# Kernel tuning notes

Measured on AMD Instinct MI355X. Metric: run time of the kernel, lower is better.

Reference implementation:

```python
import jax, jax.numpy as jnp
import numpy as np

# ---------------- config (from ObjectDetector source) ----------------
B = 2; IMG = 224; STRIDE = 32; FH = IMG // STRIDE          # 7x7 feature map
C_FEAT = 1024
SIZES = (32., 64., 128., 256., 512.); RATIOS = (0.5, 1.0, 2.0)
A = len(SIZES) * len(RATIOS)                                # 15 anchors/loc
NA = FH * FH * A                                            # 735 anchors/img
PRE_NMS = min(1000, NA); POST_NMS = min(1000, NA)           # testing config
RPN_NMS_T = 0.7; RPN_MIN_SIZE = 1e-3
NUM_CLASSES = 37
ROI_OUT = 7; ROI_SR = 2; ROI_SCALE = 1.0 / STRIDE
REP = 1024
SCORE_T = 0.05; DET_NMS_T = 0.5; DETS_PER_IMG = 100
CAND_K = 2048            # candidate cap before final batched NMS
MIN_SIZE_DET = 1e-2
BBOX_CLIP = float(np.log(1000.0 / 16.0))


def make_anchors():
    scales = np.array(SIZES, np.float32); ratios = np.array(RATIOS, np.float32)
    h_r = np.sqrt(ratios); w_r = 1.0 / h_r
    ws = (w_r[:, None] * scales[None, :]).reshape(-1)
    hs = (h_r[:, None] * scales[None, :]).reshape(-1)
    base = np.round(np.stack([-ws, -hs, ws, hs], 1) / 2.0)   # [A,4]
    sy, sx = np.meshgrid(np.arange(FH) * STRIDE, np.arange(FH) * STRIDE, indexing='ij')
    shifts = np.stack([sx.reshape(-1), sy.reshape(-1), sx.reshape(-1), sy.reshape(-1)], 1).astype(np.float32)
    return jnp.asarray((shifts[:, None, :] + base[None, :, :]).reshape(-1, 4))  # [NA,4] (H,W,A)


def conv(x, w, b, stride=1, pad=0):
    y = jax.lax.conv_general_dilated(x, w, (stride, stride), [(pad, pad)] * 2,
                                     dimension_numbers=('NCHW', 'OIHW', 'NCHW'))
    return y + b[None, :, None, None]


def decode_boxes(deltas, boxes, weights):
    wx, wy, ww, wh = weights
    w = boxes[..., 2] - boxes[..., 0]; h = boxes[..., 3] - boxes[..., 1]
    cx = boxes[..., 0] + 0.5 * w; cy = boxes[..., 1] + 0.5 * h
    dx = deltas[..., 0] / wx; dy = deltas[..., 1] / wy
    dw = jnp.minimum(deltas[..., 2] / ww, BBOX_CLIP)
    dh = jnp.minimum(deltas[..., 3] / wh, BBOX_CLIP)
    pcx = dx * w + cx; pcy = dy * h + cy
    pw = jnp.exp(dw) * w; ph = jnp.exp(dh) * h
    return jnp.stack([pcx - 0.5 * pw, pcy - 0.5 * ph, pcx + 0.5 * pw, pcy + 0.5 * ph], -1)


def clip_boxes(b):
    x = jnp.clip(b[..., 0::2], 0.0, float(IMG)); y = jnp.clip(b[..., 1::2], 0.0, float(IMG))
    return jnp.stack([x[..., 0], y[..., 0], x[..., 1], y[..., 1]], -1)


def box_iou(a, b):
    area_a = (a[:, 2] - a[:, 0]) * (a[:, 3] - a[:, 1])
    area_b = (b[:, 2] - b[:, 0]) * (b[:, 3] - b[:, 1])
    lt = jnp.maximum(a[:, None, :2], b[None, :, :2])
    rb = jnp.minimum(a[:, None, 2:], b[None, :, 2:])
    wh = jnp.clip(rb - lt, 0.0, None)
    inter = wh[..., 0] * wh[..., 1]
    return inter / jnp.maximum(area_a[:, None] + area_b[None, :] - inter, 1e-9)


def nms_keep(boxes, scores, thresh):
    """Greedy NMS; returns keep mask in original order (fixed shapes)."""
    n = boxes.shape[0]
    order = jnp.argsort(-scores)
    iou = box_iou(*(jax.lax.stop_gradient(boxes[order]),) * 2)
    idx = jnp.arange(n)
    def body(i, keep):
        sup = (iou[i] > thresh) & (idx > i) & keep[i]
        return keep & ~sup
    keep_sorted = jax.lax.fori_loop(0, n, body, jnp.ones(n, bool))
    return jnp.zeros(n, bool).at[order].set(keep_sorted)


def rpn_filter_one(obj_logits, deltas, anchors):
    # obj_logits [NA], deltas [NA,4] (detached, as in torchvision RPN)
    top_v, top_i = jax.lax.top_k(obj_logits, PRE_NMS)
    boxes = clip_boxes(decode_boxes(deltas[top_i], anchors[top_i], (1., 1., 1., 1.)))
    prob = jax.nn.sigmoid(top_v)
    ws = boxes[:, 2] - boxes[:, 0]; hs = boxes[:, 3] - boxes[:, 1]
    prob = jnp.where((ws >= RPN_MIN_SIZE) & (hs >= RPN_MIN_SIZE), prob, -1.0)
    prob = jnp.where(nms_keep(boxes, prob, RPN_NMS_T), prob, -1.0)
    sv, si = jax.lax.top_k(prob, POST_NMS)
    return boxes[si], sv > 0.0


def bilinear(f_hwc, ys, xs):
    # torchvision roi_align bilinear sampling; f_hwc [H,W,C], ys/xs [R,O]
    H, W, _ = f_hwc.shape
    vy = (ys >= -1.0) & (ys <= H); vx = (xs >= -1.0) & (xs <= W)
    y = jnp.clip(ys, 0.0, None); x = jnp.clip(xs, 0.0, None)
    y0 = jnp.minimum(jnp.floor(y).astype(jnp.int32), H - 1)
    x0 = jnp.minimum(jnp.floor(x).astype(jnp.int32), W - 1)
    y1 = jnp.minimum(y0 + 1, H - 1); x1 = jnp.minimum(x0 + 1, W - 1)
    y = jnp.where(y0 == H - 1, y0.astype(y.dtype), y)
    x = jnp.where(x0 == W - 1, x0.astype(x.dtype), x)
    ly = y - y0; lx = x - x0; hy = 1.0 - ly; hx = 1.0 - lx
    g = lambda yi, xi: f_hwc[yi[:, :, None], xi[:, None, :]]   # [R,O,O,C]
    val = ((hy[:, :, None] * hx[:, None, :])[..., None] * g(y0, x0)
         + (hy[:, :, None] * lx[:, None, :])[..., None] * g(y0, x1)
         + (ly[:, :, None] * hx[:, None, :])[..., None] * g(y1, x0)
         + (ly[:, :, None] * lx[:, None, :])[..., None] * g(y1, x1))
    return val * (vy[:, :, None] & vx[:, None, :])[..., None]


def roi_align_one(feat_chw, rois):
    # feat [C,H,W], rois [R,4] -> [R,C,7,7]; output_size=7, sampling_ratio=2, scale=1/32
    f = jnp.transpose(feat_chw, (1, 2, 0))
    x1 = rois[:, 0] * ROI_SCALE; y1 = rois[:, 1] * ROI_SCALE
    rw = jnp.maximum(rois[:, 2] * ROI_SCALE - x1, 1.0)
    rh = jnp.maximum(rois[:, 3] * ROI_SCALE - y1, 1.0)
    bw = rw / ROI_OUT; bh = rh / ROI_OUT
    grid = jnp.arange(ROI_OUT, dtype=jnp.float32)
    acc = 0.0
    for iy in range(ROI_SR):
        ys = y1[:, None] + (grid[None, :] + (iy + 0.5) / ROI_SR) * bh[:, None]
        for ix in range(ROI_SR):
            xs = x1[:, None] + (grid[None, :] + (ix + 0.5) / ROI_SR) * bw[:, None]
            acc = acc + bilinear(f, ys, xs)
    return jnp.transpose(acc / (ROI_SR * ROI_SR), (0, 3, 1, 2))


def postprocess_one(logits, box_deltas, proposals, roi_valid):
    R = logits.shape[0]
    scores = jax.nn.softmax(logits, -1)
    boxes = clip_boxes(decode_boxes(box_deltas.reshape(R, NUM_CLASSES, 4),
                                    proposals[:, None, :], (10., 10., 5., 5.)))
    boxes = boxes[:, 1:, :].reshape(-1, 4)       # drop background class
    scores = jnp.where(roi_valid[:, None], scores[:, 1:], 0.0).reshape(-1)
    labels = jnp.broadcast_to(jnp.arange(1, NUM_CLASSES)[None, :], (R, NUM_CLASSES - 1)).reshape(-1)
    ws = boxes[:, 2] - boxes[:, 0]; hs = boxes[:, 3] - boxes[:, 1]
    ok = (ws >= MIN_SIZE_DET) & (hs >= MIN_SIZE_DET) & (scores > SCORE_T)
    cs, ci = jax.lax.top_k(jnp.where(ok, scores, -1.0), CAND_K)
    cb = boxes[ci]; cl = labels[ci]
    off = cl.astype(cb.dtype) * (IMG + 1.0)      # batched (per-class) NMS trick
    keep = nms_keep(cb + off[:, None], cs, DET_NMS_T)
    tv, ti = jax.lax.top_k(jnp.where(keep, cs, -1.0), DETS_PER_IMG)
    valid = tv > 0.0
    out_boxes = jnp.where(valid[:, None], cb[ti], 0.0)
    out_scores = jnp.where(valid, tv, 0.0)
    out_labels = jnp.where(valid, cl[ti], 0).astype(out_boxes.dtype)
    return jnp.concatenate([out_boxes, out_scores[:, None], out_labels[:, None]], -1)  # [100,6]


def forward(images, params, anchors):
    (bb_w, bb_b, rpn_w, rpn_b, cls_w, cls_b, reg_w, reg_b,
     fc1_w, fc1_b, fc2_w, fc2_b, clsp_w, clsp_b, boxp_w, boxp_b) = params
    Bn = images.shape[0]
    feats = jax.nn.relu(conv(images, bb_w, bb_b, stride=STRIDE))        # [B,1024,7,7]
    t = jax.nn.relu(conv(feats, rpn_w, rpn_b, stride=1, pad=1))
    obj = jnp.transpose(conv(t, cls_w, cls_b), (0, 2, 3, 1)).reshape(Bn, -1)            # [B,NA]
    reg = jnp.transpose(conv(t, reg_w, reg_b).reshape(Bn, A, 4, FH, FH),
                        (0, 3, 4, 1, 2)).reshape(Bn, -1, 4)                              # [B,NA,4]
    obj_d = jax.lax.stop_gradient(obj); reg_d = jax.lax.stop_gradient(reg)  # RPN detaches
    proposals, roi_valid = jax.vmap(lambda o, d: rpn_filter_one(o, d, anchors))(obj_d, reg_d)
    pooled = jax.vmap(roi_align_one)(feats, proposals)                  # [B,R,1024,7,7]
    x = pooled.reshape(Bn * POST_NMS, -1)
    x = jax.nn.relu(x @ fc1_w.T + fc1_b)
    x = jax.nn.relu(x @ fc2_w.T + fc2_b)
    logits = (x @ clsp_w.T + clsp_b).reshape(Bn, POST_NMS, NUM_CLASSES)
    bdelt = (x @ boxp_w.T + boxp_b).reshape(Bn, POST_NMS, NUM_CLASSES * 4)
    return jax.vmap(postprocess_one)(logits, bdelt, proposals, roi_valid)  # [B,100,6]


def setup_inputs() -> dict:
    key = jax.random.key(0)
    ks = jax.random.split(key, 10)
    w = lambda k, shape, s=0.02: jax.random.normal(k, shape, jnp.float32) * s
    return {
        'images': jax.random.uniform(ks[0], (B, 1, IMG, IMG), jnp.float32),
        'bb_w': w(ks[1], (C_FEAT, 1, STRIDE, STRIDE)), 'bb_b': jnp.zeros((C_FEAT,), jnp.float32),
        'rpn_w': w(ks[2], (C_FEAT, C_FEAT, 3, 3)), 'rpn_b': jnp.zeros((C_FEAT,), jnp.float32),
        'cls_w': w(ks[3], (A, C_FEAT, 1, 1)), 'cls_b': jnp.zeros((A,), jnp.float32),
        'reg_w': w(ks[4], (4 * A, C_FEAT, 1, 1)), 'reg_b': jnp.zeros((4 * A,), jnp.float32),
        'fc1_w': w(ks[5], (REP, C_FEAT * ROI_OUT * ROI_OUT), 0.005), 'fc1_b': jnp.zeros((REP,), jnp.float32),
        'fc2_w': w(ks[6], (REP, REP)), 'fc2_b': jnp.zeros((REP,), jnp.float32),
        'clsp_w': w(ks[7], (NUM_CLASSES, REP)), 'clsp_b': jnp.zeros((NUM_CLASSES,), jnp.float32),
        'boxp_w': w(ks[8], (NUM_CLASSES * 4, REP)), 'boxp_b': jnp.zeros((NUM_CLASSES * 4,), jnp.float32),
    }


def reference(images, bb_w, bb_b, rpn_w, rpn_b, cls_w, cls_b, reg_w, reg_b,
              fc1_w, fc1_b, fc2_w, fc2_b, clsp_w, clsp_b, boxp_w, boxp_b):
    anchors = make_anchors()
    params = (bb_w, bb_b, rpn_w, rpn_b, cls_w, cls_b, reg_w, reg_b,
              fc1_w, fc1_b, fc2_w, fc2_b, clsp_w, clsp_b, boxp_w, boxp_b)
    return forward(images, params, anchors)
```

## Files before the change

kernel.cpp:

```cpp
#include <hip/hip_runtime.h>
#include <math.h>

#define NANCH 735
#define NCAND 26460
#define NCANDP 26624
#define BBCLIP 4.135166556742356f
#define KF1 4864
#define KHALF 2432

typedef short bf16x8 __attribute__((ext_vector_type(8)));
typedef float f32x4 __attribute__((ext_vector_type(4)));

__device__ __forceinline__ unsigned short f2b(float f) {
  unsigned int u = __float_as_uint(f);
  unsigned int r = (u >> 16) & 1u;
  u += 0x7fffu + r;
  return (unsigned short)(u >> 16);
}

__device__ __forceinline__ void anchor_of(int i, float* o) {
  int pos = i / 15, a = i % 15;
  int iy = pos / 7, ix = pos % 7;
  int rr = a / 5, sc = a % 5;
  double ratio = (rr == 0) ? 0.5 : (rr == 1 ? 1.0 : 2.0);
// ... 12 lines not shown

template<int NTOT, int NTH>
__device__ void bitonic_sort_sh(float* v, int* id) {
  const int t = threadIdx.x;
  for (int k = 2; k <= NTOT; k <<= 1) {
    for (int j = k >> 1; j > 0; j >>= 1) {
      for (int s = t; s < NTOT; s += NTH) {
        int p = s ^ j;
        if (p > s) {
          float v1 = v[s], v2 = v[p];
          int i1 = id[s], i2 = id[p];
          bool up = ((s & k) == 0);
          if (before_(v2, i2, v1, i1) == up) {
            v[s] = v2; id[s] = i2; v[p] = v1; id[p] = i1;
          }
        }
      }
      __syncthreads();
    }
  }
}

template<int NTOT, int NTH>
__device__ void bitonic_merge_sh(float* v, int* id) {
  const int t = threadIdx.x;
  for (int j = NTOT >> 1; j > 0; j >>= 1) {
    for (int s = t; s < NTOT; s += NTH) {
      int p = s ^ j;
      if (p > s) {
        float v1 = v[s], v2 = v[p];
        int i1 = id[s], i2 = id[p];
        if (before_(v2, i2, v1, i1)) {
          v[s] = v2; id[s] = i2; v[p] = v1; id[p] = i1;
        }
      }
    }
    __syncthreads();
  }
}

__global__ void k_im2col_bb(const float* __restrict__ images, unsigned short* __restrict__ patch) {
  int i = blockIdx.x * 256 + threadIdx.x;
  if (i >= 98 * 1024) return;
  int rowi = i >> 10, k = i & 1023;
  int b = rowi / 49, pos = rowi % 49;
  int oy = pos / 7, ox = pos % 7;
  int ky = k >> 5, kx = k & 31;
  patch[i] = f2b(images[((size_t)b * 224 + oy * 32 + ky) * 224 + ox * 32 + kx]);
}

__global__ void k_im2col_rpn(const unsigned short* __restrict__ bbh,
                             unsigned short* __restrict__ im2) {
  int i = blockIdx.x * 256 + threadIdx.x;
  if (i >= 98 * 9216) return;
  int rowi = i / 9216, k = i % 9216;
  int b = rowi / 49, pos = rowi % 49;
  int oy = pos / 7, ox = pos % 7;
  int ic = k / 9, kk = k % 9;
  int ky = kk / 3, kx = kk % 3;
  int y = oy + ky - 1, x = ox + kx - 1;
  unsigned short v = 0;
  if ((unsigned)y < 7u && (unsigned)x < 7u)
    v = bbh[((size_t)(b * 49 + y * 7 + x)) * 1024 + ic];
  im2[i] = v;
}

__global__ __launch_bounds__(256) void k_gemm_bf16(
    const unsigned short* __restrict__ A, int lda, int M,
    const unsigned short* __restrict__ B, int ldb,
    float* __restrict__ P, int N, int Kchunk,
    const int* __restrict__ nvalid)
{
  __shared__ __attribute__((aligned(16))) unsigned short As[2][128][40];
  __shared__ __attribute__((aligned(16))) unsigned short Bs[2][128][40];
  const int G = gridDim.x * gridDim.y * gridDim.z;
  int lid = blockIdx.x + gridDim.x * (blockIdx.y + gridDim.y * blockIdx.z);
  lid = (lid & 7) * (G >> 3) + (lid >> 3);
  const int bx = lid % gridDim.x;
  const int rest = lid / gridDim.x;
  const int by = rest % gridDim.y, bz = rest / gridDim.y;
  const int m0 = bx * 128, n0 = by * 128;
  if (nvalid) {
    int nv0 = nvalid[0], nv1 = nvalid[1];
    bool ok = (m0 < nv0) || ((m0 + 128 > NANCH) && (m0 < NANCH + nv1));
    if (!ok) return;
  }
  const int t = threadIdx.x;
  const int lane = t & 63, wid = t >> 6;
  const int wm = (wid >> 1) * 64, wn = (wid & 1) * 64;
  const size_t k0 = (size_t)bz * Kchunk;
  f32x4 acc[4][4];
#pragma unroll
  for (int i = 0; i < 4; ++i)
#pragma unroll
    for (int j = 0; j < 4; ++j) acc[i][j] = (f32x4){0.f, 0.f, 0.f, 0.f};
  const int r0 = t >> 2, c0 = (t & 3) * 8;
  const int fr = lane & 15, fk = (lane >> 4) * 8;
  const int gmA0 = m0 + r0, gmA1 = m0 + r0 + 64;
  const bool vA0 = gmA0 < M, vA1 = gmA1 < M;
  const unsigned short* pA0 = A + (size_t)gmA0 * lda + k0 + c0;
  const unsigned short* pA1 = A + (size_t)gmA1 * lda + k0 + c0;
  const unsigned short* pB0 = B + (size_t)(n0 + r0) * ldb + k0 + c0;
  const unsigned short* pB1 = B + (size_t)(n0 + r0 + 64) * ldb + k0 + c0;
  bf16x8 rA0 = {}, rA1 = {}, rB0, rB1;
  if (vA0) rA0 = *(const bf16x8*)pA0;
  if (vA1) rA1 = *(const bf16x8*)pA1;
  rB0 = *(const bf16x8*)pB0;
  rB1 = *(const bf16x8*)pB1;
  const int nt = Kchunk >> 5;
  int cur = 0;
  for (int it = 0; it < nt; ++it) {
    *(bf16x8*)&As[cur][r0][c0] = rA0;
    *(bf16x8*)&As[cur][r0 + 64][c0] = rA1;
    *(bf16x8*)&Bs[cur][r0][c0] = rB0;
    *(bf16x8*)&Bs[cur][r0 + 64][c0] = rB1;
    __syncthreads();
    if (it + 1 < nt) {
      size_t ofs = (size_t)(it + 1) * 32;
      rA0 = vA0 ? *(const bf16x8*)(pA0 + ofs) : (bf16x8){};
      rA1 = vA1 ? *(const bf16x8*)(pA1 + ofs) : (bf16x8){};
      rB0 = *(const bf16x8*)(pB0 + ofs);
      rB1 = *(const bf16x8*)(pB1 + ofs);
    }
    bf16x8 af[4], bg[4];
#pragma unroll
    for (int i = 0; i < 4; ++i) af[i] = *(const bf16x8*)&As[cur][wm + i * 16 + fr][fk];
#pragma unroll
    for (int j = 0; j < 4; ++j) bg[j] = *(const bf16x8*)&Bs[cur][wn + j * 16 + fr][fk];
#pragma unroll
    for (int i = 0; i < 4; ++i)
#pragma unroll
      for (int j = 0; j < 4; ++j)
        acc[i][j] = __builtin_amdgcn_mfma_f32_16x16x32_bf16(af[i], bg[j], acc[i][j], 0, 0, 0);
    cur ^= 1;
  }
  float* Pp = P + (size_t)bz * M * N;
#pragma unroll
  for (int i = 0; i < 4; ++i) {
#pragma unroll
    for (int r = 0; r < 4; ++r) {
      int gm = m0 + wm + i * 16 + (lane >> 4) * 4 + r;
      if (gm < M) {
#pragma unroll
        for (int j = 0; j < 4; ++j)
          Pp[(size_t)gm * N + n0 + wn + j * 16 + (lane & 15)] = acc[i][j][r];
      }
    }
  }
}

__global__ __launch_bounds__(256) void k_gemm_mb(
    const unsigned short* __restrict__ A,
    const unsigned short* __restrict__ W1p,
    unsigned short* __restrict__ Mbh)
{
  __shared__ __attribute__((aligned(16))) unsigned short As[2][128][40];
  __shared__ __attribute__((aligned(16))) unsigned short Bs[2][128][40];
  const int G = gridDim.x * gridDim.y * gridDim.z;
  int lid = blockIdx.x + gridDim.x * (blockIdx.y + gridDim.y * blockIdx.z);
  lid = (lid & 7) * (G >> 3) + (lid >> 3);
  const int rest = lid;
  const int by = rest % gridDim.y, p = rest / gridDim.y;
  const int n0 = by * 128;
  const int M = 98;
  const unsigned short* B = W1p + (size_t)p * 1048576;
  const int t = threadIdx.x;
  const int lane = t & 63, wid = t >> 6;
  const int wm = (wid >> 1) * 64, wn = (wid & 1) * 64;
  f32x4 acc[4][4];
#pragma unroll
  for (int i = 0; i < 4; ++i)
#pragma unroll
    for (int j = 0; j < 4; ++j) acc[i][j] = (f32x4){0.f, 0.f, 0.f, 0.f};
  const int r0 = t >> 2, c0 = (t & 3) * 8;
  const int fr = lane & 15, fk = (lane >> 4) * 8;
  int gA0 = r0; if (gA0 >= M) gA0 = M - 1;
  int gA1 = r0 + 64; if (gA1 >= M) gA1 = M - 1;
  const unsigned short* pA0 = A + (size_t)gA0 * 1024 + c0;
  const unsigned short* pA1 = A + (size_t)gA1 * 1024 + c0;
  const unsigned short* pB0 = B + (size_t)(n0 + r0) * 1024 + c0;
  const unsigned short* pB1 = B + (size_t)(n0 + r0 + 64) * 1024 + c0;
  bf16x8 rA0 = *(const bf16x8*)pA0;
  bf16x8 rA1 = *(const bf16x8*)pA1;
  bf16x8 rB0 = *(const bf16x8*)pB0;
  bf16x8 rB1 = *(const bf16x8*)pB1;
  const int nt = 1024 >> 5;
  int cur = 0;
  for (int it = 0; it < nt; ++it) {
    *(bf16x8*)&As[cur][r0][c0] = rA0;
    *(bf16x8*)&As[cur][r0 + 64][c0] = rA1;
    *(bf16x8*)&Bs[cur][r0][c0] = rB0;
    *(bf16x8*)&Bs[cur][r0 + 64][c0] = rB1;
    __syncthreads();
    if (it + 1 < nt) {
      size_t ofs = (size_t)(it + 1) * 32;
      rA0 = *(const bf16x8*)(pA0 + ofs);
      rA1 = *(const bf16x8*)(pA1 + ofs);
      rB0 = *(const bf16x8*)(pB0 + ofs);
      rB1 = *(const bf16x8*)(pB1 + ofs);
    }
    bf16x8 af[4], bg[4];
#pragma unroll
    for (int i = 0; i < 4; ++i) af[i] = *(const bf16x8*)&As[cur][wm + i * 16 + fr][fk];
#pragma unroll
    for (int j = 0; j < 4; ++j) bg[j] = *(const bf16x8*)&Bs[cur][wn + j * 16 + fr][fk];
#pragma unroll
    for (int i = 0; i < 4; ++i)
#pragma unroll
      for (int j = 0; j < 4; ++j)
        acc[i][j] = __builtin_amdgcn_mfma_f32_16x16x32_bf16(af[i], bg[j], acc[i][j], 0, 0, 0);
    cur ^= 1;
  }
  unsigned short* Pp = Mbh + (size_t)p * 98 * 1024;
#pragma unroll
  for (int i = 0; i < 4; ++i) {
#pragma unroll
    for (int r = 0; r < 4; ++r) {
      int gm = wm + i * 16 + (lane >> 4) * 4 + r;
      if (gm < M) {
#pragma unroll
        for (int j = 0; j < 4; ++j)
          Pp[(size_t)gm * 1024 + n0 + wn + j * 16 + (lane & 15)] = f2b(acc[i][j][r]);
      }
    }
  }
}

__global__ __launch_bounds__(256) void k_mtrans(const unsigned short* __restrict__ Mbh,
                                                unsigned short* __restrict__ Bmat)
{
  __shared__ unsigned short tile[98][129];
  const int p = blockIdx.x, n0 = blockIdx.y * 128;
  const int t = threadIdx.x;
  for (int j = t; j < 98 * 128; j += 256) {
    int q = j >> 7, nl = j & 127;
    tile[q][nl] = Mbh[((size_t)p * 98 + q) * 1024 + n0 + nl];
  }
  __syncthreads();
  for (int j = t; j < 128 * 98; j += 256) {
    int nl = j / 98, q2 = j % 98;
    int bb = q2 >= 49 ? 1 : 0;
    int col = bb * KHALF + p * 49 + (q2 - bb * 49);
    Bmat[(size_t)(n0 + nl) * KF1 + col] = tile[q2][nl];
  }
  if (p == 0) {
    for (int j = t; j < 128 * 62; j += 256) {
      int nl = j / 62, e = j % 62;
      int bb = e >= 31 ? 1 : 0;
      int col = bb * KHALF + 2401 + (e - bb * 31);
      Bmat[(size_t)(n0 + nl) * KF1 + col] = 0;
    }
  }
}

__global__ __launch_bounds__(256) void k_gbuild(const float* __restrict__ props,
                                                unsigned short* __restrict__ Gmat)
{
#pragma clang fp contract(off)
  int rg = blockIdx.x;
  int b = rg / NANCH;
  __shared__ float g[KF1];
  int t = threadIdx.x;
  for (int j = t; j < KF1; j += 256) g[j] = 0.f;
  __syncthreads();
  if (t < 49) {
    const float* roi = props + (size_t)rg * 4;
    int p = t, oy = p / 7, ox = p % 7;
    float x1 = roi[0] * 0.03125f, y1 = roi[1] * 0.03125f;
    float rw = fmaxf(roi[2] * 0.03125f - x1, 1.f);
    float rh = fmaxf(roi[3] * 0.03125f - y1, 1.f);
    float bw = rw / 7.f, bh = rh / 7.f;
    float* gb = g + b * KHALF + p * 49;
    for (int iy = 0; iy < 2; ++iy) {
      for (int ix = 0; ix < 2; ++ix) {
        float ys = y1 + ((float)oy + ((float)iy + 0.5f) * 0.5f) * bh;
        float xs = x1 + ((float)ox + ((float)ix + 0.5f) * 0.5f) * bw;
        bool vy = (ys >= -1.f) && (ys <= 7.f);
        bool vx = (xs >= -1.f) && (xs <= 7.f);
        float yc = fmaxf(ys, 0.f), xc = fmaxf(xs, 0.f);
        int y0 = min((int)floorf(yc), 6), x0 = min((int)floorf(xc), 6);
        int y1i = min(y0 + 1, 6), x1i = min(x0 + 1, 6);
        if (y0 == 6) yc = 6.f;
        if (x0 == 6) xc = 6.f;
        float ly = yc - (float)y0, lx = xc - (float)x0;
        float hy = 1.f - ly, hx = 1.f - lx;
        float vm = (vy && vx) ? 0.25f : 0.f;
        gb[y0 * 7 + x0]   += hy * hx * vm;
        gb[y0 * 7 + x1i]  += hy * lx * vm;
        gb[y1i * 7 + x0]  += ly * hx * vm;
        gb[y1i * 7 + x1i] += ly * lx * vm;
      }
    }
  }
  __syncthreads();
  unsigned short* Gr = Gmat + (size_t)rg * KF1;
  for (int j = t; j < KF1; j += 256) Gr[j] = f2b(g[j]);
}

__global__ void k_reduce(const float* __restrict__ P, float* __restrict__ dst,
                         unsigned short* __restrict__ dst16,
                         int S, int M, int N, const float* __restrict__ bias, int flags)
{
  size_t i = (size_t)blockIdx.x * 256 + threadIdx.x;
  size_t tot = (size_t)M * N;
  if (i >= tot) return;
  float v = (flags & 1) ? 0.f : dst[i];
  for (int s = 0; s < S; ++s) v += P[(size_t)s * tot + i];
  if (flags & 2) v += bias[i % (size_t)N];
  if (flags & 4) v = fmaxf(v, 0.f);
  if (!(flags & 16)) dst[i] = v;
  if (flags & 8) dst16[i] = f2b(v);
}

__global__ void k_f2b3(const float* __restrict__ s1, unsigned short* __restrict__ d1,
                       const float* __restrict__ s2, unsigned short* __restrict__ d2,
                       const float* __restrict__ s3, unsigned short* __restrict__ d3)
{
  int i = (blockIdx.x * 256 + threadIdx.x) * 4;
  const float* s; unsigned short* d; int off;
  if (i < 1048576) { s = s1; d = d1; off = i; }
  else if (i < 2097152) { s = s2; d = d2; off = i - 1048576; }
  else if (i < 11534336) { s = s3; d = d3; off = i - 2097152; }
  else return;
  float4 v = *(const float4*)(s + off);
  ushort4 o;
  o.x = f2b(v.x); o.y = f2b(v.y); o.z = f2b(v.z); o.w = f2b(v.w);
  *(ushort4*)(d + off) = o;
}

__global__ __launch_bounds__(256) void k_w1perm2(const float* __restrict__ w,
                                                 unsigned short* __restrict__ o)
{
  __shared__ unsigned short tile[128 * 50];
  const int n = blockIdx.x, ct = blockIdx.y;
  const float* src = w + (size_t)n * 50176 + (size_t)ct * 128 * 49;
  const int t = threadIdx.x;
  for (int i = t; i < 6272; i += 256) {
    int cl = i / 49, p = i % 49;
    tile[cl * 50 + p] = f2b(src[i]);
  }
  __syncthreads();
  for (int j = t; j < 6272; j += 256) {
    int p = j >> 7, cl = j & 127;
    o[((size_t)p * 1024 + n) * 1024 + (size_t)ct * 128 + cl] = tile[cl * 50 + p];
  }
}

__global__ __launch_bounds__(256) void k_rpn_head(
    const float* __restrict__ tmn, const float* __restrict__ cls_w,
    const float* __restrict__ cls_b, const float* __restrict__ reg_w,
    const float* __restrict__ reg_b, float* __restrict__ obj, float* __restrict__ reg)
{
  int blk = blockIdx.x;
  __shared__ float col[1024];
  const float* row = tmn + (size_t)blk * 1024;
  for (int i = threadIdx.x; i < 1024; i += 256) col[i] = row[i];
  __syncthreads();
  int b = blk / 49, pos = blk % 49;
  for (int o = threadIdx.x; o < 75; o += 256) {
    const float* w = (o < 15) ? (cls_w + (size_t)o * 1024) : (reg_w + (size_t)(o - 15) * 1024);
    float s = 0.f;
    for (int k = 0; k < 1024; ++k) s = fmaf(col[k], w[k], s);
    if (o < 15) {
      obj[(size_t)b * NANCH + pos * 15 + o] = s + cls_b[o];
    } else {
      int c = o - 15, a = c >> 2, d = c & 3;
      reg[((size_t)b * NANCH + pos * 15 + a) * 4 + d] = s + reg_b[c];
    }
  }
}

__global__ __launch_bounds__(1024) void k_rpn_prep(
    const float* __restrict__ obj, const float* __restrict__ reg,
    float* __restrict__ bxp, float* __restrict__ pnms)
{
#pragma clang fp contract(off)
  const int b = blockIdx.x, t = threadIdx.x;
  __shared__ float sval[1024];
  __shared__ float vo1[1024];
  __shared__ int o1a[1024];
  __shared__ int wtv[16];
  __shared__ int wti[16];
  sval[t] = (t < NANCH) ? obj[(size_t)b * NANCH + t] : -INFINITY;
  __syncthreads();
  {
    float v = sval[t];
    int rank = 0;
    for (int j = 0; j < NANCH; ++j) {
      float u = sval[j];
      rank += (u > v) || (u == v && j < t);
    }
    if (t < NANCH) { vo1[rank] = v; o1a[rank] = t; }
  }
  __syncthreads();
  float x1 = 0.f, y1 = 0.f, x2 = 0.f, y2 = 0.f, prob = -1.f;
  bool flag = false;
  if (t < NANCH) {
    int ai = o1a[t];
    const float* d = reg + ((size_t)b * NANCH + ai) * 4;
    float an[4];
    anchor_of(ai, an);
    float aw = an[2] - an[0], ah = an[3] - an[1];
    float acx = an[0] + 0.5f * aw, acy = an[1] + 0.5f * ah;
    float dw = fminf(d[2], BBCLIP), dh = fminf(d[3], BBCLIP);
    float pcx = d[0] * aw + acx, pcy = d[1] * ah + acy;
    float pw = expf(dw) * aw, ph = expf(dh) * ah;
    x1 = pcx - 0.5f * pw; y1 = pcy - 0.5f * ph;
    x2 = pcx + 0.5f * pw; y2 = pcy + 0.5f * ph;
    x1 = fminf(fmaxf(x1, 0.f), 224.f);
    y1 = fminf(fmaxf(y1, 0.f), 224.f);
    x2 = fminf(fmaxf(x2, 0.f), 224.f);
    y2 = fminf(fmaxf(y2, 0.f), 224.f);
    flag = (x2 - x1 >= 1e-3f) && (y2 - y1 >= 1e-3f);
    prob = 1.f / (1.f + expf(-vo1[t]));
  }
  bool iflag = (t < NANCH) && !flag;
  unsigned long long balv = __ballot(flag);
  unsigned long long bali = __ballot(iflag);
  int lane = t & 63, w = t >> 6;
  if (lane == 0) { wtv[w] = __popcll(balv); wti[w] = __popcll(bali); }
  __syncthreads();
  int nval = 0, basev = 0, basei = 0;
  for (int k = 0; k < 16; ++k) {
    int cv = wtv[k], ci = wti[k];
    nval += cv;
    if (k < w) { basev += cv; basei += ci; }
  }
  if (t < NANCH) {
    unsigned long long lm = (1ull << lane) - 1;
    int pos = flag ? (basev + __popcll(balv & lm))
                   : (nval + basei + __popcll(bali & lm));
    float* o = bxp + ((size_t)b * NANCH + pos) * 4;
    o[0] = x1; o[1] = y1; o[2] = x2; o[3] = y2;
    pnms[(size_t)b * NANCH + pos] = flag ? prob : -1.f;
  }
}

__global__ __launch_bounds__(256) void k_rpn_mask(
    const float* __restrict__ bxp, unsigned long long* __restrict__ rmask)
{
#pragma clang fp contract(off)
  int blk = blockIdx.x;
  int b = blk / 35;
  int row = (blk % 35) * 21 + (int)(threadIdx.x / 12);
  int w = threadIdx.x % 12;
  if (threadIdx.x >= 252 || row >= NANCH) return;
  const float* a = bxp + ((size_t)b * NANCH + row) * 4;
  float a0 = a[0], a1 = a[1], a2 = a[2], a3 = a[3];
  float aarea = (a2 - a0) * (a3 - a1);
  int l0 = w * 64;
  int l1 = (l0 + 64 < NANCH) ? l0 + 64 : NANCH;
  int ls = (l0 > row + 1) ? l0 : row + 1;
  unsigned long long bits = 0ull;
  for (int l = ls; l < l1; ++l) {
    const float* q = bxp + ((size_t)b * NANCH + l) * 4;
    float b0 = q[0], b1 = q[1], b2 = q[2], b3 = q[3];
    float barea = (b2 - b0) * (b3 - b1);
    float ix1 = fmaxf(a0, b0), iy1 = fmaxf(a1, b1);
    float ix2 = fminf(a2, b2), iy2 = fminf(a3, b3);
    float iw = fmaxf(ix2 - ix1, 0.f), ih = fmaxf(iy2 - iy1, 0.f);
    float inter = iw * ih;
    float iou = inter / fmaxf(aarea + barea - inter, 1e-9f);
    if (iou > 0.7f) bits |= 1ull << (l & 63);
  }
  rmask[((size_t)b * NANCH + row) * 12 + w] = bits;
}

__global__ __launch_bounds__(1024) void k_rpn_fin(
    const float* __restrict__ bxp, const float* __restrict__ pnms,
    const unsigned long long* __restrict__ rmask,
    float* __restrict__ props, int* __restrict__ meta)
{
  const int b = blockIdx.x, t = threadIdx.x;
  __shared__ unsigned long long smask[NANCH * 12];
  __shared__ float sp[1024];
  __shared__ unsigned long long keepw[12];
  __shared__ int wtot[16];
  for (int i = t; i < NANCH * 12; i += 1024)
    smask[i] = rmask[(size_t)b * NANCH * 12 + i];
  sp[t] = (t < NANCH) ? pnms[(size_t)b * NANCH + t] : -1.f;
  __syncthreads();
  if (t < 64) {
    unsigned long long kl = (t < 12) ? ~0ull : 0ull;
    for (int i = 0; i < NANCH; ++i) {
      unsigned long long kw = __shfl(kl, i >> 6);
      unsigned long long m = (t < 12) ? smask[i * 12 + t] : 0ull;
      bool on = (kw >> (i & 63)) & 1ull;
      kl &= on ? ~m : ~0ull;
    }
    if (t < 12) keepw[t] = kl;
  }
  __syncthreads();
  bool flag = false;
  if (t < NANCH) {
    bool kp = (keepw[t >> 6] >> (t & 63)) & 1ull;
    flag = kp && (sp[t] > 0.f);
  }
  unsigned long long bal = __ballot(flag);
  int lane = t & 63, w = t >> 6;
  if (lane == 0) wtot[w] = __popcll(bal);
  __syncthreads();
  int base = 0, tot = 0;
  for (int k = 0; k < 16; ++k) { int c = wtot[k]; if (k < w) base += c; tot += c; }
  if (flag) {
    int pos = base + __popcll(bal & ((1ull << lane) - 1));
    const float* src = bxp + ((size_t)b * NANCH + t) * 4;
    float* o = props + ((size_t)b * NANCH + pos) * 4;
    o[0] = src[0]; o[1] = src[1]; o[2] = src[2]; o[3] = src[3];
  }
  if (t == 0) meta[b] = tot;
}

__global__ __launch_bounds__(256) void k_headcand(
    const float* __restrict__ h2, const float* __restrict__ cw,
    const float* __restrict__ cb, const float* __restrict__ bw_,
    const float* __restrict__ bb_, const int* __restrict__ meta,
    const float* __restrict__ props,
    float* __restrict__ cscore, float* __restrict__ cbox)
{
#pragma clang fp contract(off)
  int rg = blockIdx.x;
  int b = rg / NANCH, r = rg % NANCH;
  float* cs = cscore + (size_t)b * NCANDP;
  float* cbx = cbox + (size_t)b * NCANDP * 4;
  int base = r * 36;
  if (r >= meta[b]) {
    int j = threadIdx.x;
    if (j < 36) {
      cs[base + j] = -1.f;
      float* q = cbx + (size_t)(base + j) * 4;
      q[0] = 0.f; q[1] = 0.f; q[2] = 0.f; q[3] = 0.f;
    }
    return;
  }
  __shared__ float row[1024];
  __shared__ float lg[37];
  __shared__ float bd[148];
  __shared__ float mxsum[2];
  for (int i = threadIdx.x; i < 1024; i += 256) row[i] = h2[(size_t)rg * 1024 + i];
  __syncthreads();
  for (int o = threadIdx.x; o < 185; o += 256) {
    const float* w = (o < 37) ? (cw + (size_t)o * 1024) : (bw_ + (size_t)(o - 37) * 1024);
    float s = 0.f;
    for (int k = 0; k < 1024; ++k) s = fmaf(row[k], w[k], s);
    if (o < 37) lg[o] = s + cb[o];
    else bd[o - 37] = s + bb_[o - 37];
  }
  __syncthreads();
  if (threadIdx.x == 0) {
    float mx = lg[0];
    for (int c = 1; c < 37; ++c) mx = fmaxf(mx, lg[c]);
    float sum = 0.f;
    for (int c = 0; c < 37; ++c) sum += expf(lg[c] - mx);
    mxsum[0] = mx; mxsum[1] = sum;
  }
  __syncthreads();
  int c = threadIdx.x + 1;
  if (c <= 36) {
    const float* roi = props + (size_t)rg * 4;
    float rw = roi[2] - roi[0], rh = roi[3] - roi[1];
    float rcx = roi[0] + 0.5f * rw, rcy = roi[1] + 0.5f * rh;
    const float* d = bd + c * 4;
    float dx = d[0] / 10.f, dy = d[1] / 10.f;
    float dw = fminf(d[2] / 5.f, BBCLIP), dh = fminf(d[3] / 5.f, BBCLIP);
    float pcx = dx * rw + rcx, pcy = dy * rh + rcy;
    float pw = expf(dw) * rw, ph = expf(dh) * rh;
    float x1 = pcx - 0.5f * pw, y1 = pcy - 0.5f * ph;
    float x2 = pcx + 0.5f * pw, y2 = pcy + 0.5f * ph;
    x1 = fminf(fmaxf(x1, 0.f), 224.f);
    y1 = fminf(fmaxf(y1, 0.f), 224.f);
    x2 = fminf(fmaxf(x2, 0.f), 224.f);
    y2 = fminf(fmaxf(y2, 0.f), 224.f);
    float sc = expf(lg[c] - mxsum[0]) / mxsum[1];
    bool ok = ((x2 - x1) >= 1e-2f) && ((y2 - y1) >= 1e-2f) && (sc > 0.05f);
    cs[base + c - 1] = ok ? sc : -1.f;
    float* q = cbx + (size_t)(base + c - 1) * 4;
    q[0] = x1; q[1] = y1; q[2] = x2; q[3] = y2;
  }
}

__global__ __launch_bounds__(1024) void k_top2048(
    const float* __restrict__ cscore,
    float* __restrict__ sel_score, int* __restrict__ sel_cidx,
    int* __restrict__ meta)
{
  const int b = blockIdx.x, t = threadIdx.x;
  __shared__ float Lv[2048]; __shared__ int Li[2048];
  __shared__ float Cv[2048]; __shared__ int Ci[2048];
  __shared__ int cnt;
  const float* cs = cscore + (size_t)b * NCANDP;
  if (t == 0) cnt = 0;
  __syncthreads();
  for (int gi = t; gi < NCAND; gi += 1024) {
    float v = cs[gi];
    if (v > 0.f) {
      int p = atomicAdd(&cnt, 1);
      if (p < 2048) { Cv[p] = v; Ci[p] = gi; }
    }
  }
  __syncthreads();
  int npos = cnt;
  if (npos <= 2048) {
    for (int h = 0; h < 2; ++h) {
      int p = h * 1024 + t;
      if (p < npos) {
        float v = Cv[p]; int id = Ci[p];
        int rank = 0;
        for (int j = 0; j < npos; ++j) {
          float u = Cv[j]; int ju = Ci[j];
          rank += (u > v) || (u == v && ju < id);
        }
        sel_score[b * 2048 + rank] = v;
        sel_cidx[b * 2048 + rank] = id;
      }
      if (p >= npos && p < 2048) {
        sel_score[b * 2048 + p] = -1.f;
        sel_cidx[b * 2048 + p] = 0;
      }
    }
    if (t == 0) meta[2 + b] = npos;
    return;
  }
  for (int chunk = 0; chunk < 13; ++chunk) {
    for (int s = t; s < 2048; s += 1024) {
      int gi = chunk * 2048 + s;
      Cv[s] = (gi < NCAND) ? cs[gi] : -INFINITY;
      Ci[s] = gi;
    }
    __syncthreads();
    bitonic_sort_sh<2048, 1024>(Cv, Ci);
    if (chunk == 0) {
      for (int s = t; s < 2048; s += 1024) { Lv[s] = Cv[s]; Li[s] = Ci[s]; }
      __syncthreads();
    } else {
      for (int s = t; s < 2048; s += 1024) {
        float cv = Cv[2047 - s]; int ci = Ci[2047 - s];
        if (before_(cv, ci, Lv[s], Li[s])) { Lv[s] = cv; Li[s] = ci; }
      }
      __syncthreads();
      bitonic_merge_sh<2048, 1024>(Lv, Li);
    }
  }
  for (int s = t; s < 2048; s += 1024) {
    sel_score[b * 2048 + s] = Lv[s];
    sel_cidx[b * 2048 + s] = Li[s];
  }
  if (t == 0) meta[2 + b] = 2048;
}

__global__ void k_detmask(const int* __restrict__ sel_cidx,
                          const float* __restrict__ cbox,
                          const int* __restrict__ meta,
                          unsigned long long* __restrict__ dmask)
{
#pragma clang fp contract(off)
  int blk = blockIdx.x;
  int b = blk >> 8, row0 = (blk & 255) * 8;
  int npos = meta[2 + b];
  if (row0 >= npos) return;
  int t = threadIdx.x;
  int i = row0 + (t >> 5), w = t & 31;
  if (i >= npos) return;
  int ci = sel_cidx[b * 2048 + i];
  const float* bp = cbox + ((size_t)b * NCANDP + ci) * 4;
  float off = (float)(ci % 36 + 1) * 225.f;
  float a0 = bp[0] + off, a1 = bp[1] + off, a2 = bp[2] + off, a3 = bp[3] + off;
  float aarea = (a2 - a0) * (a3 - a1);
  unsigned long long bits = 0ull;
  int l0 = w * 64;
  int l1 = (l0 + 64 < npos) ? l0 + 64 : npos;
  int ls = (l0 > i + 1) ? l0 : i + 1;
  for (int l = ls; l < l1; ++l) {
    int cl = sel_cidx[b * 2048 + l];
    const float* q = cbox + ((size_t)b * NCANDP + cl) * 4;
    float o2 = (float)(cl % 36 + 1) * 225.f;
    float b0 = q[0] + o2, b1 = q[1] + o2, b2 = q[2] + o2, b3 = q[3] + o2;
    float barea = (b2 - b0) * (b3 - b1);
    float ix1 = fmaxf(a0, b0), iy1 = fmaxf(a1, b1);
    float ix2 = fminf(a2, b2), iy2 = fminf(a3, b3);
    float iw = fmaxf(ix2 - ix1, 0.f), ih = fmaxf(iy2 - iy1, 0.f);
    float inter = iw * ih;
    float iou = inter / fmaxf(aarea + barea - inter, 1e-9f);
    if (iou > 0.5f) bits |= 1ull << (l & 63);
  }
  dmask[((size_t)b * 2048 + i) * 32 + w] = bits;
}

__global__ __launch_bounds__(1024) void k_final(
    const float* __restrict__ sel_score, const int* __restrict__ sel_cidx,
    const float* __restrict__ cbox, const unsigned long long* __restrict__ dmask,
    const int* __restrict__ meta, float* __restrict__ out)
{
  const int b = blockIdx.x, t = threadIdx.x;
  __shared__ unsigned long long keepw[32];
  __shared__ float sv[2048];
  __shared__ float kv[2048]; __shared__ int ks[2048];
  __shared__ int wtot[32];
  int npos = meta[2 + b];
  for (int h = 0; h < 2; ++h) {
    int s = h * 1024 + t;
    sv[s] = sel_score[b * 2048 + s];
  }
  __syncthreads();
  if (t < 64) {
    unsigned long long kl = (t < 32) ? ~0ull : 0ull;
    for (int i = 0; i < npos; ++i) {
      unsigned long long kw = __shfl(kl, i >> 6);
      unsigned long long m = (t < 32) ? dmask[((size_t)b * 2048 + i) * 32 + t] : 0ull;
      bool on = (kw >> (i & 63)) & 1ull;
      kl &= on ? ~m : ~0ull;
    }
    if (t < 32) keepw[t] = kl;
  }
  __syncthreads();
  const int lane = t & 63, w = t >> 6;
  int s0 = t;
  bool f0 = ((keepw[s0 >> 6] >> (s0 & 63)) & 1ull) && (sv[s0] > 0.f);
  unsigned long long bal0 = __ballot(f0);
  if (lane == 0) wtot[w] = __popcll(bal0);
  int s1 = 1024 + t;
  bool f1 = ((keepw[s1 >> 6] >> (s1 & 63)) & 1ull) && (sv[s1] > 0.f);
  unsigned long long bal1 = __ballot(f1);
  if (lane == 0) wtot[16 + w] = __popcll(bal1);
  __syncthreads();
  int nk = 0, base0 = 0, base1 = 0;
  for (int k = 0; k < 32; ++k) {
    int c = wtot[k];
    if (k < w) base0 += c;
    if (k < 16 + w) base1 += c;
    nk += c;
  }
  int p0 = -1, p1 = -1;
  if (f0) { p0 = base0 + __popcll(bal0 & ((1ull << lane) - 1)); kv[p0] = sv[s0]; ks[p0] = s0; }
  if (f1) { p1 = base1 + __popcll(bal1 & ((1ull << lane) - 1)); kv[p1] = sv[s1]; ks[p1] = s1; }
  __syncthreads();
  if (f0) {
    float v = sv[s0]; int rank = 0;
    for (int j = 0; j < nk; ++j) { float u = kv[j]; int ju = ks[j]; rank += (u > v) || (u == v && ju < s0); }
    if (rank < 100) {
      int ci = sel_cidx[b * 2048 + s0];
      const float* bp = cbox + ((size_t)b * NCANDP + ci) * 4;
      float* o = out + ((size_t)b * 100 + rank) * 6;
      o[0] = bp[0]; o[1] = bp[1]; o[2] = bp[2]; o[3] = bp[3];
      o[4] = v; o[5] = (float)(ci % 36 + 1);
    }
  }
  if (f1) {
    float v = sv[s1]; int rank = 0;
    for (int j = 0; j < nk; ++j) { float u = kv[j]; int ju = ks[j]; rank += (u > v) || (u == v && ju < s1); }
    if (rank < 100) {
      int ci = sel_cidx[b * 2048 + s1];
      const float* bp = cbox + ((size_t)b * NCANDP + ci) * 4;
      float* o = out + ((size_t)b * 100 + rank) * 6;
      o[0] = bp[0]; o[1] = bp[1]; o[2] = bp[2]; o[3] = bp[3];
      o[4] = v; o[5] = (float)(ci % 36 + 1);
    }
  }
  if (t < 100 && t >= nk) {
    float* o = out + ((size_t)b * 100 + t) * 6;
    o[0] = 0.f; o[1] = 0.f; o[2] = 0.f; o[3] = 0.f; o[4] = 0.f; o[5] = 0.f;
  }
}

extern "C" void kernel_launch(void* const* d_in, const int* in_sizes, int n_in,
                              void* d_out, int out_size, void* d_ws, size_t ws_size,
                              hipStream_t stream)
{
  (void)in_sizes; (void)n_in; (void)out_size; (void)ws_size;
  const float* images = (const float*)d_in[0];
  const float* bb_w   = (const float*)d_in[1];
  const float* bb_b   = (const float*)d_in[2];
  const float* rpn_w  = (const float*)d_in[3];
  const float* rpn_b  = (const float*)d_in[4];
  const float* cls_w  = (const float*)d_in[5];
  const float* cls_b  = (const float*)d_in[6];
  const float* reg_w  = (const float*)d_in[7];
  const float* reg_b  = (const float*)d_in[8];
  const float* fc1_w  = (const float*)d_in[9];
  const float* fc1_b  = (const float*)d_in[10];
  const float* fc2_w  = (const float*)d_in[11];
  const float* fc2_b  = (const float*)d_in[12];
  const float* clsp_w = (const float*)d_in[13];
  const float* clsp_b = (const float*)d_in[14];
  const float* boxp_w = (const float*)d_in[15];
  const float* boxp_b = (const float*)d_in[16];
  float* out = (float*)d_out;
  char* ws = (char*)d_ws;

  size_t off = 0;
  auto alloc = [&](size_t bytes) -> size_t {
    size_t o = off; off = (off + bytes + 255) & ~(size_t)255; return o;
  };
  size_t o_patch = alloc(98ull * 1024 * 2);
  size_t o_bbC   = alloc(98ull * 1024 * 4);
  size_t o_bbh   = alloc(98ull * 1024 * 2);
  size_t o_t     = alloc(98ull * 1024 * 4);
  size_t o_im2   = alloc(98ull * 9216 * 2);
  size_t o_obj   = alloc(1470ull * 4);
  size_t o_reg   = alloc(1470ull * 16);
  size_t o_props = alloc(1470ull * 16);
  size_t o_bxp   = alloc(1470ull * 16);
  size_t o_pnms  = alloc(1470ull * 4);
  size_t o_rm    = alloc(1470ull * 12 * 8);
  size_t o_meta  = alloc(256);
  size_t o_y1    = alloc(1470ull * 1024 * 4);
  size_t o_y2    = alloc(1470ull * 1024 * 4);
  size_t o_cs    = alloc(2ull * NCANDP * 4);
  size_t o_cb    = alloc(2ull * NCANDP * 16);
  size_t o_ss    = alloc(2ull * 2048 * 4);
  size_t o_sc    = alloc(2ull * 2048 * 4);
  size_t o_dm    = alloc(2ull * 2048 * 32 * 8);
  size_t o_w0b   = alloc(1048576ull * 2);
  size_t o_w3b   = alloc(9437184ull * 2);
  size_t o_w1p   = alloc(51380224ull * 2);
  size_t o_mbh   = alloc(49ull * 98 * 1024 * 2);
  size_t o_bmat  = alloc(1024ull * KF1 * 2);
  size_t o_gmat  = alloc(1470ull * KF1 * 2);
  size_t o_w2b   = alloc(1048576ull * 2);
  size_t o_y1b   = alloc(1470ull * 1024 * 2);
  size_t o_P     = alloc(32ull * 98 * 1024 * 4 > 4ull * 1470 * 1024 * 4
                         ? 32ull * 98 * 1024 * 4 : 4ull * 1470 * 1024 * 4);

  unsigned short* patchb = (unsigned short*)(ws + o_patch);
  float* bbC   = (float*)(ws + o_bbC);
  unsigned short* bbh = (unsigned short*)(ws + o_bbh);
  float* tb    = (float*)(ws + o_t);
  unsigned short* im2b = (unsigned short*)(ws + o_im2);
  float* objb  = (float*)(ws + o_obj);
  float* regb  = (float*)(ws + o_reg);
  float* props = (float*)(ws + o_props);
  float* bxp   = (float*)(ws + o_bxp);
  float* pnms  = (float*)(ws + o_pnms);
  unsigned long long* rmb = (unsigned long long*)(ws + o_rm);
  int*   meta  = (int*)(ws + o_meta);
  float* y1    = (float*)(ws + o_y1);
  float* y2    = (float*)(ws + o_y2);
  float* csb   = (float*)(ws + o_cs);
  float* cbb   = (float*)(ws + o_cb);
  float* ssb   = (float*)(ws + o_ss);
  int*   scb   = (int*)(ws + o_sc);
  unsigned long long* dmb = (unsigned long long*)(ws + o_dm);
  unsigned short* w0b = (unsigned short*)(ws + o_w0b);
  unsigned short* w3b = (unsigned short*)(ws + o_w3b);
  unsigned short* w1p = (unsigned short*)(ws + o_w1p);
  unsigned short* mbh = (unsigned short*)(ws + o_mbh);
  unsigned short* bmat = (unsigned short*)(ws + o_bmat);
  unsigned short* gmat = (unsigned short*)(ws + o_gmat);
  unsigned short* w2b = (unsigned short*)(ws + o_w2b);
  unsigned short* y1b = (unsigned short*)(ws + o_y1b);
  float* Pb    = (float*)(ws + o_P);

  k_w1perm2<<<dim3(1024, 8), 256, 0, stream>>>(fc1_w, w1p);
  k_f2b3<<<11264, 256, 0, stream>>>(fc2_w, w2b, bb_w, w0b, rpn_w, w3b);
  k_im2col_bb<<<392, 256, 0, stream>>>(images, patchb);
  k_gemm_bf16<<<dim3(1, 8, 8), 256, 0, stream>>>(patchb, 1024, 98, w0b, 1024, Pb, 1024, 128, nullptr);
  k_reduce<<<392, 256, 0, stream>>>(Pb, bbC, bbh, 8, 98, 1024, bb_b, 31);
  k_gemm_mb<<<dim3(1, 8, 49), 256, 0, stream>>>(bbh, w1p, mbh);
  k_mtrans<<<dim3(49, 8), 256, 0, stream>>>(mbh, bmat);
  k_im2col_rpn<<<3528, 256, 0, stream>>>(bbh, im2b);
  k_gemm_bf16<<<dim3(1, 8, 32), 256, 0, stream>>>(im2b, 9216, 98, w3b, 9216, Pb, 1024, 288, nullptr);
  k_reduce<<<392, 256, 0, stream>>>(Pb, tb, nullptr, 32, 98, 1024, rpn_b, 7);
  k_rpn_head<<<98, 256, 0, stream>>>(tb, cls_w, cls_b, reg_w, reg_b, objb, regb);
  k_rpn_prep<<<2, 1024, 0, stream>>>(objb, regb, bxp, pnms);
  k_rpn_mask<<<70, 256, 0, stream>>>(bxp, rmb);
  k_rpn_fin<<<2, 1024, 0, stream>>>(bxp, pnms, rmb, props, meta);
  k_gbuild<<<1470, 256, 0, stream>>>(props, gmat);
  k_gemm_bf16<<<dim3(12, 8, 4), 256, 0, stream>>>(gmat, KF1, 1470, bmat, KF1, Pb, 1024, 1216, meta);
  k_reduce<<<5880, 256, 0, stream>>>(Pb, y1, y1b, 4, 1470, 1024, fc1_b, 31);
  k_gemm_bf16<<<dim3(12, 8, 2), 256, 0, stream>>>(y1b, 1024, 1470, w2b, 1024, Pb, 1024, 512, meta);
  k_reduce<<<5880, 256, 0, stream>>>(Pb, y2, nullptr, 2, 1470, 1024, fc2_b, 7);
  k_headcand<<<1470, 256, 0, stream>>>(y2, clsp_w, clsp_b, boxp_w, boxp_b, meta, props, csb, cbb);
  k_top2048<<<2, 1024, 0, stream>>>(csb, ssb, scb, meta);
  k_detmask<<<512, 256, 0, stream>>>(scb, cbb, meta, dmb);
  k_final<<<2, 1024, 0, stream>>>(ssb, scb, cbb, dmb, meta, out);
}
```

Measured before the change: 457.8 us.

## Fuse fc1 transpose into GEMM epilogue and run box head as bf16 MFMA GEMM

The fc1 weight-projection GEMM now stages its bf16 output in shared memory and writes the transposed Bmat layout directly, which removes the separate k_mtrans kernel and its intermediate buffer. The class and box predictor heads, previously a scalar per-ROI dot-product loop in k_headcand, are now a padded 256-column bf16 MFMA GEMM with split-K. The bf16 head weights are produced in the existing conversion kernel, and a light per-ROI kernel finishes softmax and box decoding. This trades fp32 head precision for bf16 and adds an extra GEMM launch, while the strided column writes in the fused epilogue may be poorly coalesced.

```diff
diff --git a/kernel.cpp b/kernel.cpp
--- a/kernel.cpp
+++ b/kernel.cpp
@@ -188,10 +188,11 @@
 __global__ __launch_bounds__(256) void k_gemm_mb(
     const unsigned short* __restrict__ A,
     const unsigned short* __restrict__ W1p,
-    unsigned short* __restrict__ Mbh)
+    unsigned short* __restrict__ Bmat)
 {
   __shared__ __attribute__((aligned(16))) unsigned short As[2][128][40];
   __shared__ __attribute__((aligned(16))) unsigned short Bs[2][128][40];
+  __shared__ unsigned short tile[98][130];
   const int G = gridDim.x * gridDim.y * gridDim.z;
   int lid = blockIdx.x + gridDim.x * (blockIdx.y + gridDim.y * blockIdx.z);
   lid = (lid & 7) * (G >> 3) + (lid >> 3);
@@ -247,7 +248,7 @@
         acc[i][j] = __builtin_amdgcn_mfma_f32_16x16x32_bf16(af[i], bg[j], acc[i][j], 0, 0, 0);
     cur ^= 1;
   }
-  unsigned short* Pp = Mbh + (size_t)p * 98 * 1024;
+  __syncthreads();
 #pragma unroll
   for (int i = 0; i < 4; ++i) {
 #pragma unroll
@@ -256,32 +257,19 @@
       if (gm < M) {
 #pragma unroll
         for (int j = 0; j < 4; ++j)
-          Pp[(size_t)gm * 1024 + n0 + wn + j * 16 + (lane & 15)] = f2b(acc[i][j][r]);
+          tile[gm][wn + j * 16 + (lane & 15)] = f2b(acc[i][j][r]);
       }
     }
   }
-}
-
-__global__ __launch_bounds__(256) void k_mtrans(const unsigned short* __restrict__ Mbh,
-                                                unsigned short* __restrict__ Bmat)
-{
-  __shared__ unsigned short tile[98][129];
-  const int p = blockIdx.x, n0 = blockIdx.y * 128;
-  const int t = threadIdx.x;
-  for (int j = t; j < 98 * 128; j += 256) {
-    int q = j >> 7, nl = j & 127;
-    tile[q][nl] = Mbh[((size_t)p * 98 + q) * 1024 + n0 + nl];
-  }
-  __syncthreads();
-  for (int j = t; j < 128 * 98; j += 256) {
-    int nl = j / 98, q2 = j % 98;
-    int bb = q2 >= 49 ? 1 : 0;
-    int col = bb * KHALF + p * 49 + (q2 - bb * 49);
-    Bmat[(size_t)(n0 + nl) * KF1 + col] = tile[q2][nl];
+  __syncthreads();
+  {
+    int nl = t >> 1, b2 = t & 1;
+    unsigned short* dst = Bmat + (size_t)(n0 + nl) * KF1 + b2 * KHALF + p * 49;
+    for (int qq = 0; qq < 49; ++qq) dst[qq] = tile[b2 * 49 + qq][nl];
   }
   if (p == 0) {
-    for (int j = t; j < 128 * 62; j += 256) {
-      int nl = j / 62, e = j % 62;
+    for (int j2 = t; j2 < 128 * 62; j2 += 256) {
+      int nl = j2 / 62, e = j2 % 62;
       int bb = e >= 31 ? 1 : 0;
       int col = bb * KHALF + 2401 + (e - bb * 31);
       Bmat[(size_t)(n0 + nl) * KF1 + col] = 0;
@@ -350,13 +338,31 @@
 
 __global__ void k_f2b3(const float* __restrict__ s1, unsigned short* __restrict__ d1,
                        const float* __restrict__ s2, unsigned short* __restrict__ d2,
-                       const float* __restrict__ s3, unsigned short* __restrict__ d3)
+                       const float* __restrict__ s3, unsigned short* __restrict__ d3,
+                       const float* __restrict__ cw, const float* __restrict__ bw,
+                       unsigned short* __restrict__ d4)
 {
   int i = (blockIdx.x * 256 + threadIdx.x) * 4;
   const float* s; unsigned short* d; int off;
   if (i < 1048576) { s = s1; d = d1; off = i; }
   else if (i < 2097152) { s = s2; d = d2; off = i - 1048576; }
   else if (i < 11534336) { s = s3; d = d3; off = i - 2097152; }
+  else if (i < 11796480) {
+    int off4 = i - 11534336;
+    int row = off4 >> 10, col = off4 & 1023;
+    ushort4 o;
+    if (row < 37) {
+      float4 v = *(const float4*)(cw + (size_t)row * 1024 + col);
+      o.x = f2b(v.x); o.y = f2b(v.y); o.z = f2b(v.z); o.w = f2b(v.w);
+    } else if (row < 185) {
+      float4 v = *(const float4*)(bw + (size_t)(row - 37) * 1024 + col);
+      o.x = f2b(v.x); o.y = f2b(v.y); o.z = f2b(v.z); o.w = f2b(v.w);
+    } else {
+      o.x = 0; o.y = 0; o.z = 0; o.w = 0;
+    }
+    *(ushort4*)(d4 + off4) = o;
+    return;
+  }
   else return;
   float4 v = *(const float4*)(s + off);
   ushort4 o;
@@ -547,58 +553,44 @@
   if (t == 0) meta[b] = tot;
 }
 
-__global__ __launch_bounds__(256) void k_headcand(
-    const float* __restrict__ h2, const float* __restrict__ cw,
-    const float* __restrict__ cb, const float* __restrict__ bw_,
-    const float* __restrict__ bb_, const int* __restrict__ meta,
-    const float* __restrict__ props,
-    float* __restrict__ cscore, float* __restrict__ cbox)
+__global__ void k_cand(const float* __restrict__ P, const float* __restrict__ cb_,
+                       const float* __restrict__ bb_, const float* __restrict__ props,
+                       const int* __restrict__ meta,
+                       float* __restrict__ cscore, float* __restrict__ cbox)
 {
 #pragma clang fp contract(off)
-  int rg = blockIdx.x;
+  int rg = blockIdx.x * blockDim.x + threadIdx.x;
+  if (rg >= 2 * NANCH) return;
   int b = rg / NANCH, r = rg % NANCH;
   float* cs = cscore + (size_t)b * NCANDP;
   float* cbx = cbox + (size_t)b * NCANDP * 4;
   int base = r * 36;
   if (r >= meta[b]) {
-    int j = threadIdx.x;
-    if (j < 36) {
+    for (int j = 0; j < 36; ++j) {
       cs[base + j] = -1.f;
       float* q = cbx + (size_t)(base + j) * 4;
       q[0] = 0.f; q[1] = 0.f; q[2] = 0.f; q[3] = 0.f;
     }
     return;
   }
-  __shared__ float row[1024];
-  __shared__ float lg[37];
-  __shared__ float bd[148];
-  __shared__ float mxsum[2];
-  for (int i = threadIdx.x; i < 1024; i += 256) row[i] = h2[(size_t)rg * 1024 + i];
-  __syncthreads();
-  for (int o = threadIdx.x; o < 185; o += 256) {
-    const float* w = (o < 37) ? (cw + (size_t)o * 1024) : (bw_ + (size_t)(o - 37) * 1024);
-    float s = 0.f;
-    for (int k = 0; k < 1024; ++k) s = fmaf(row[k], w[k], s);
-    if (o < 37) lg[o] = s + cb[o];
-    else bd[o - 37] = s + bb_[o - 37];
-  }
-  __syncthreads();
-  if (threadIdx.x == 0) {
-    float mx = lg[0];
-    for (int c = 1; c < 37; ++c) mx = fmaxf(mx, lg[c]);
-    float sum = 0.f;
-    for (int c = 0; c < 37; ++c) sum += expf(lg[c] - mx);
-    mxsum[0] = mx; mxsum[1] = sum;
-  }
-  __syncthreads();
-  int c = threadIdx.x + 1;
-  if (c <= 36) {
-    const float* roi = props + (size_t)rg * 4;
-    float rw = roi[2] - roi[0], rh = roi[3] - roi[1];
-    float rcx = roi[0] + 0.5f * rw, rcy = roi[1] + 0.5f * rh;
-    const float* d = bd + c * 4;
-    float dx = d[0] / 10.f, dy = d[1] / 10.f;
-    float dw = fminf(d[2] / 5.f, BBCLIP), dh = fminf(d[3] / 5.f, BBCLIP);
+  const float* p0 = P + (size_t)rg * 256;
+  const float* p1 = P + 1470ull * 256 + (size_t)rg * 256;
+  float lg[37];
+  for (int c = 0; c < 37; ++c) lg[c] = p0[c] + p1[c] + cb_[c];
+  float mx = lg[0];
+  for (int c = 1; c < 37; ++c) mx = fmaxf(mx, lg[c]);
+  float sum = 0.f;
+  for (int c = 0; c < 37; ++c) sum += expf(lg[c] - mx);
+  const float* roi = props + (size_t)rg * 4;
+  float rw = roi[2] - roi[0], rh = roi[3] - roi[1];
+  float rcx = roi[0] + 0.5f * rw, rcy = roi[1] + 0.5f * rh;
+  for (int c = 1; c < 37; ++c) {
+    float d0 = p0[37 + c * 4]     + p1[37 + c * 4]     + bb_[c * 4];
+    float d1 = p0[37 + c * 4 + 1] + p1[37 + c * 4 + 1] + bb_[c * 4 + 1];
+    float d2 = p0[37 + c * 4 + 2] + p1[37 + c * 4 + 2] + bb_[c * 4 + 2];
+    float d3 = p0[37 + c * 4 + 3] + p1[37 + c * 4 + 3] + bb_[c * 4 + 3];
+    float dx = d0 / 10.f, dy = d1 / 10.f;
+    float dw = fminf(d2 / 5.f, BBCLIP), dh = fminf(d3 / 5.f, BBCLIP);
     float pcx = dx * rw + rcx, pcy = dy * rh + rcy;
     float pw = expf(dw) * rw, ph = expf(dh) * rh;
     float x1 = pcx - 0.5f * pw, y1 = pcy - 0.5f * ph;
@@ -607,7 +599,7 @@
     y1 = fminf(fmaxf(y1, 0.f), 224.f);
     x2 = fminf(fmaxf(x2, 0.f), 224.f);
     y2 = fminf(fmaxf(y2, 0.f), 224.f);
-    float sc = expf(lg[c] - mxsum[0]) / mxsum[1];
+    float sc = expf(lg[c] - mx) / sum;
     bool ok = ((x2 - x1) >= 1e-2f) && ((y2 - y1) >= 1e-2f) && (sc > 0.05f);
     cs[base + c - 1] = ok ? sc : -1.f;
     float* q = cbx + (size_t)(base + c - 1) * 4;
@@ -849,11 +841,12 @@
   size_t o_w0b   = alloc(1048576ull * 2);
   size_t o_w3b   = alloc(9437184ull * 2);
   size_t o_w1p   = alloc(51380224ull * 2);
-  size_t o_mbh   = alloc(49ull * 98 * 1024 * 2);
   size_t o_bmat  = alloc(1024ull * KF1 * 2);
   size_t o_gmat  = alloc(1470ull * KF1 * 2);
   size_t o_w2b   = alloc(1048576ull * 2);
+  size_t o_hwb   = alloc(256ull * 1024 * 2);
   size_t o_y1b   = alloc(1470ull * 1024 * 2);
+  size_t o_y2b   = alloc(1470ull * 1024 * 2);
   size_t o_P     = alloc(32ull * 98 * 1024 * 4 > 4ull * 1470 * 1024 * 4
                          ? 32ull * 98 * 1024 * 4 : 4ull * 1470 * 1024 * 4);
 
@@ -870,7 +863,6 @@
   unsigned long long* rmb = (unsigned long long*)(ws + o_rm);
   int*   meta  = (int*)(ws + o_meta);
   float* y1    = (float*)(ws + o_y1);
-  float* y2    = (float*)(ws + o_y2);
   float* csb   = (float*)(ws + o_cs);
   float* cbb   = (float*)(ws + o_cb);
   float* ssb   = (float*)(ws + o_ss);
@@ -879,20 +871,20 @@
   unsigned short* w0b = (unsigned short*)(ws + o_w0b);
   unsigned short* w3b = (unsigned short*)(ws + o_w3b);
   unsigned short* w1p = (unsigned short*)(ws + o_w1p);
-  unsigned short* mbh = (unsigned short*)(ws + o_mbh);
   unsigned short* bmat = (unsigned short*)(ws + o_bmat);
   unsigned short* gmat = (unsigned short*)(ws + o_gmat);
   unsigned short* w2b = (unsigned short*)(ws + o_w2b);
+  unsigned short* hwb = (unsigned short*)(ws + o_hwb);
   unsigned short* y1b = (unsigned short*)(ws + o_y1b);
+  unsigned short* y2b = (unsigned short*)(ws + o_y2b);
   float* Pb    = (float*)(ws + o_P);
 
   k_w1perm2<<<dim3(1024, 8), 256, 0, stream>>>(fc1_w, w1p);
-  k_f2b3<<<11264, 256, 0, stream>>>(fc2_w, w2b, bb_w, w0b, rpn_w, w3b);
+  k_f2b3<<<11520, 256, 0, stream>>>(fc2_w, w2b, bb_w, w0b, rpn_w, w3b, clsp_w, boxp_w, hwb);
   k_im2col_bb<<<392, 256, 0, stream>>>(images, patchb);
   k_gemm_bf16<<<dim3(1, 8, 8), 256, 0, stream>>>(patchb, 1024, 98, w0b, 1024, Pb, 1024, 128, nullptr);
   k_reduce<<<392, 256, 0, stream>>>(Pb, bbC, bbh, 8, 98, 1024, bb_b, 31);
-  k_gemm_mb<<<dim3(1, 8, 49), 256, 0, stream>>>(bbh, w1p, mbh);
-  k_mtrans<<<dim3(49, 8), 256, 0, stream>>>(mbh, bmat);
+  k_gemm_mb<<<dim3(1, 8, 49), 256, 0, stream>>>(bbh, w1p, bmat);
   k_im2col_rpn<<<3528, 256, 0, stream>>>(bbh, im2b);
   k_gemm_bf16<<<dim3(1, 8, 32), 256, 0, stream>>>(im2b, 9216, 98, w3b, 9216, Pb, 1024, 288, nullptr);
   k_reduce<<<392, 256, 0, stream>>>(Pb, tb, nullptr, 32, 98, 1024, rpn_b, 7);
@@ -904,8 +896,9 @@
   k_gemm_bf16<<<dim3(12, 8, 4), 256, 0, stream>>>(gmat, KF1, 1470, bmat, KF1, Pb, 1024, 1216, meta);
   k_reduce<<<5880, 256, 0, stream>>>(Pb, y1, y1b, 4, 1470, 1024, fc1_b, 31);
   k_gemm_bf16<<<dim3(12, 8, 2), 256, 0, stream>>>(y1b, 1024, 1470, w2b, 1024, Pb, 1024, 512, meta);
-  k_reduce<<<5880, 256, 0, stream>>>(Pb, y2, nullptr, 2, 1470, 1024, fc2_b, 7);
-  k_headcand<<<1470, 256, 0, stream>>>(y2, clsp_w, clsp_b, boxp_w, boxp_b, meta, props, csb, cbb);
+  k_reduce<<<5880, 256, 0, stream>>>(Pb, y1, y2b, 2, 1470, 1024, fc2_b, 31);
+  k_gemm_bf16<<<dim3(12, 2, 2), 256, 0, stream>>>(y2b, 1024, 1470, hwb, 1024, Pb, 256, 512, meta);
+  k_cand<<<6, 256, 0, stream>>>(Pb, clsp_b, boxp_b, props, meta, csb, cbb);
   k_top2048<<<2, 1024, 0, stream>>>(csb, ssb, scb, meta);
   k_detmask<<<512, 256, 0, stream>>>(scb, cbb, meta, dmb);
   k_final<<<2, 1024, 0, stream>>>(ssb, scb, cbb, dmb, meta, out);
```

Result: no change. 455.1 us (-0.6%).
